# Optimization experiments

Hardware: AMD Instinct MI355X
Metric: run time of the kernel (lower is better)

Reference implementation:

```python
import jax, jax.numpy as jnp
import numpy as np

N_NODES = 50000
N_EDGES = 800000
HID = 64


def fake_quant_w(w):
    # symmetric per-tensor int8 fake quantization (num_bits=8)
    s = jnp.maximum(jnp.max(jnp.abs(w)) / 127.0, 1e-8)
    q = jnp.clip(jnp.round(w / s), -127.0, 127.0) * s
    return w + jax.lax.stop_gradient(q - w)


def layer_norm(x, g, b, eps=1e-5):
    mu = jnp.mean(x, axis=-1, keepdims=True)
    var = jnp.var(x, axis=-1, keepdims=True)
    return (x - mu) * jax.lax.rsqrt(var + eps) * g + b


def pointnet_conv(x, pos, src, dst, W, n_nodes):
    # message: cat([x_j, pos_j - pos_i]) @ W_q^T, max-aggregated at i (dst)
    rel = pos[src] - pos[dst]                       # [E, 3]
    feat = jnp.concatenate([x[src], rel], axis=-1)  # [E, C+3]
    msg = feat @ fake_quant_w(W).T                  # [E, 64]
    h = jax.ops.segment_max(msg, dst, num_segments=n_nodes)
    return jnp.where(jnp.isfinite(h), h, 0.0)       # empty segments -> 0


def setup_inputs() -> dict:
    key = jax.random.key(0)
    ks = jax.random.split(key, 16)
    d = {}
    d["x"] = jax.random.normal(ks[0], (N_NODES, 1), jnp.float32)
    d["pos"] = jax.random.normal(ks[1], (N_NODES, 3), jnp.float32)
    d["edge_index"] = jax.random.randint(ks[2], (2, N_EDGES), 0, N_NODES, jnp.int32)
    sc = 0.02
    d["W0"] = jax.random.normal(ks[3], (HID, 1 + 3), jnp.float32) * sc
    d["Ws"] = jax.random.normal(ks[4], (4, HID, HID + 3), jnp.float32) * sc
    d["ln_g"] = jnp.ones((5, HID), jnp.float32)
    d["ln_b"] = jnp.zeros((5, HID), jnp.float32)
    d["mlp_w1"] = jax.random.normal(ks[5], (128, 320), jnp.float32) * sc
    d["mlp_b1"] = jnp.zeros((128,), jnp.float32)
    d["mlp_w2"] = jax.random.normal(ks[6], (128, 128), jnp.float32) * sc
    d["mlp_b2"] = jnp.zeros((128,), jnp.float32)
    d["mlp_w3"] = jax.random.normal(ks[7], (64, 128), jnp.float32) * sc
    d["mlp_b3"] = jnp.zeros((64,), jnp.float32)
    d["mlp_w4"] = jax.random.normal(ks[8], (2, 64), jnp.float32) * sc
    d["mlp_b4"] = jnp.zeros((2,), jnp.float32)
    d["scale"] = jnp.ones((2,), jnp.float32)
    return d


def reference(x, pos, edge_index, W0, Ws, ln_g, ln_b,
              mlp_w1, mlp_b1, mlp_w2, mlp_b2, mlp_w3, mlp_b3, mlp_w4, mlp_b4,
              scale):
    src, dst = edge_index[0], edge_index[1]
    n = x.shape[0]
    embeddings = []
    h = x
    for i in range(5):
        W = W0 if i == 0 else Ws[i - 1]
        h = pointnet_conv(h, pos, src, dst, W, n)
        h = layer_norm(h, ln_g[i], ln_b[i])
        h = jax.nn.relu(h)
        embeddings.append(h)
    z = jnp.concatenate(embeddings, axis=-1)  # [N, 320]
    z = layer_norm(z, jnp.ones((z.shape[-1],), z.dtype), jnp.zeros((z.shape[-1],), z.dtype))
    z = jax.nn.relu(z @ mlp_w1.T + mlp_b1)
    z = jax.nn.relu(z @ mlp_w2.T + mlp_b2)
    z = jax.nn.relu(z @ mlp_w3.T + mlp_b3)
    flow = (z @ mlp_w4.T + mlp_b4) * scale
    return flow
```

## Files before the change

kernel.cpp:

```cpp
#include <hip/hip_runtime.h>
#include <hip/hip_bf16.h>

#define N_NODES 50000
#define N_EDGES 800000
#define NBLK 196

__device__ __forceinline__ float bf2f(unsigned short u) {
    union { unsigned int i; float f; } c; c.i = ((unsigned int)u) << 16; return c.f;
}
__device__ __forceinline__ unsigned short f2bf(float f) {
    union { float f; unsigned int u; } c; c.f = f;
    unsigned int u = c.u;
    u += 0x7fffu + ((u >> 16) & 1u);
    return (unsigned short)(u >> 16);
}
__device__ __forceinline__ float ldin(const void* p, long i, int f32) {
    return f32 ? ((const float*)p)[i] : bf2f(((const unsigned short*)p)[i]);
}
__device__ __forceinline__ float wsum(float v) {
#pragma unroll
    for (int m = 32; m; m >>= 1) v += __shfl_xor(v, m, 64);
    return v;
}

__global__ void probe_kernel(const unsigned short* __restrict__ lng, int* __restrict__ flag) {
    if (threadIdx.x == 0 && blockIdx.x == 0)
        flag[0] = (lng[0] == 0x3F80 && lng[1] == 0x3F80) ? 0 : 1;
}

__global__ __launch_bounds__(256) void hist_kernel(const int* __restrict__ ei, int* __restrict__ deg) {
    int e = blockIdx.x * 256 + threadIdx.x;
    if (e < N_EDGES) atomicAdd(&deg[ei[N_EDGES + e]], 1);
}

__global__ __launch_bounds__(256) void bsum_kernel(const int* __restrict__ deg,
                                                   int* __restrict__ bsum) {
    __shared__ int wt[4];
    const int t = threadIdx.x, lane = t & 63, wid = t >> 6;
    const int i = blockIdx.x * 256 + t;
    int v = (i < N_NODES) ? deg[i] : 0;
    int r = v;
#pragma unroll
    for (int m = 32; m; m >>= 1) r += __shfl_xor(r, m, 64);
    if (lane == 0) wt[wid] = r;
    __syncthreads();
    if (t == 0) bsum[blockIdx.x] = wt[0] + wt[1] + wt[2] + wt[3];
}

__global__ __launch_bounds__(256) void boff_kernel(const int* __restrict__ bsum,
                                                   int* __restrict__ boff) {
    __shared__ int wt[4];
    const int t = threadIdx.x, lane = t & 63, wid = t >> 6;
    int v = (t < NBLK) ? bsum[t] : 0;
    int inc = v;
#pragma unroll
    for (int off = 1; off < 64; off <<= 1) {
        int u = __shfl_up(inc, off, 64);
        if (lane >= off) inc += u;
    }
    if (lane == 63) wt[wid] = inc;
    __syncthreads();
    int woff = 0;
    for (int w = 0; w < wid; ++w) woff += wt[w];
    if (t < NBLK) boff[t] = inc - v + woff;
}

__global__ __launch_bounds__(256) void scanout_kernel(const int* __restrict__ deg,
                                                      const int* __restrict__ boff,
                                                      int* __restrict__ rowptr,
                                                      int* __restrict__ cursor) {
    __shared__ int wt[4];
    const int t = threadIdx.x, lane = t & 63, wid = t >> 6;
    const int i = blockIdx.x * 256 + t;
    int v = (i < N_NODES) ? deg[i] : 0;
    int inc = v;
#pragma unroll
    for (int off = 1; off < 64; off <<= 1) {
        int u = __shfl_up(inc, off, 64);
        if (lane >= off) inc += u;
    }
    if (lane == 63) wt[wid] = inc;
    __syncthreads();
    int woff = 0;
    for (int w = 0; w < wid; ++w) woff += wt[w];
    int excl = inc - v + woff + boff[blockIdx.x];
    if (i < N_NODES) {
        rowptr[i] = excl;
        cursor[i] = excl;
        if (i == N_NODES - 1) rowptr[N_NODES] = excl + v;
    }
}

__global__ __launch_bounds__(256) void scatter_kernel(const int* __restrict__ ei,
                                                      int* __restrict__ cursor,
                                                      int* __restrict__ csr_src) {
    int e = blockIdx.x * 256 + threadIdx.x;
    if (e < N_EDGES) {
        int src = ei[e];
        int dst = ei[N_EDGES + e];
        int p = atomicAdd(&cursor[dst], 1);
        csr_src[p] = src;
    }
}

__global__ __launch_bounds__(256) void quant_kernel(const void* __restrict__ W0,
                                                    const void* __restrict__ Ws,
                                                    float* __restrict__ Wc0,
                                                    float* __restrict__ Wc,
                                                    float* __restrict__ Wr,
                                                    const int* __restrict__ flagp) {
    const int f32 = *flagp;
    int layer = blockIdx.x;
    const void* src = (layer == 0) ? W0 : Ws;
    long sbase = (layer == 0) ? 0 : (long)(layer - 1) * 4288;
    float* dstc = (layer == 0) ? Wc0 : Wc + (size_t)(layer - 1) * 4352;
    float* dstr = (layer == 0) ? nullptr : Wr + (size_t)(layer - 1) * 4352;
    int Ki = (layer == 0) ? 4 : 67;
    int n = 64 * Ki;
    __shared__ float red[256];
    float amax = 0.0f;
    for (int i = threadIdx.x; i < n; i += 256) amax = fmaxf(amax, fabsf(ldin(src, sbase + i, f32)));
    red[threadIdx.x] = amax;
    __syncthreads();
    for (int s = 128; s > 0; s >>= 1) {
        if (threadIdx.x < s) red[threadIdx.x] = fmaxf(red[threadIdx.x], red[threadIdx.x + s]);
        __syncthreads();
    }
    float sc = fmaxf(red[0] / 127.0f, 1e-8f);
    for (int i = threadIdx.x; i < n; i += 256) {
        float w = ldin(src, sbase + i, f32);
        float q = rintf(w / sc);
        q = fminf(fmaxf(q, -127.0f), 127.0f);
        float v = q * sc;
        int o = i / Ki, k = i % Ki;
        dstc[(size_t)k * 64 + o] = v;
        if (dstr) dstr[(size_t)o * 68 + k] = v;
    }
}

__global__ __launch_bounds__(256) void wcvt_kernel(const void* __restrict__ w1,
                                                   const void* __restrict__ w2,
                                                   const void* __restrict__ w3,
                                                   float* __restrict__ Wm,
                                                   const int* __restrict__ flagp) {
    const int f32 = *flagp;
    const int i = blockIdx.x * 256 + threadIdx.x;
    if (i < 40960) Wm[i] = ldin(w1, i, f32);
    else if (i < 57344) Wm[i] = ldin(w2, i - 40960, f32);
    else if (i < 65536) Wm[i] = ldin(w3, i - 57344, f32);
}

__global__ __launch_bounds__(256) void u0_kernel(const void* __restrict__ x,
                                                 const void* __restrict__ pos,
                                                 const float* __restrict__ Wc0,
                                                 float* __restrict__ u,
                                                 const int* __restrict__ flagp) {
    const int f32 = *flagp;
    const int n = blockIdx.x * 256 + threadIdx.x;
    if (n >= N_NODES) return;
    const float xv = ldin(x, n, f32);
    const float p0 = ldin(pos, 3L * n + 0, f32);
    const float p1 = ldin(pos, 3L * n + 1, f32);
    const float p2 = ldin(pos, 3L * n + 2, f32);
    float4* up = reinterpret_cast<float4*>(u + (size_t)n * 64);
#pragma unroll
    for (int q = 0; q < 16; ++q) {
        const float4 w0 = *reinterpret_cast<const float4*>(Wc0 + 0 * 64 + 4 * q);
        const float4 w1 = *reinterpret_cast<const float4*>(Wc0 + 1 * 64 + 4 * q);
        const float4 w2 = *reinterpret_cast<const float4*>(Wc0 + 2 * 64 + 4 * q);
        const float4 w3 = *reinterpret_cast<const float4*>(Wc0 + 3 * 64 + 4 * q);
        float4 o;
        o.x = fmaf(p2, w3.x, fmaf(p1, w2.x, fmaf(p0, w1.x, xv * w0.x)));
        o.y = fmaf(p2, w3.y, fmaf(p1, w2.y, fmaf(p0, w1.y, xv * w0.y)));
        o.z = fmaf(p2, w3.z, fmaf(p1, w2.z, fmaf(p0, w1.z, xv * w0.z)));
        o.w = fmaf(p2, w3.w, fmaf(p1, w2.w, fmaf(p0, w1.w, xv * w0.w)));
        up[q] = o;
    }
}

__global__ __launch_bounds__(256) void agg_kernel(const float* __restrict__ u,
                                                  const void* __restrict__ pos,
                                                  const int* __restrict__ rowptr,
                                                  const int* __restrict__ csr,
                                                  const float* __restrict__ WcV, int vrow,
                                                  const void* __restrict__ lng,
                                                  const void* __restrict__ lnb,
                                                  int lnoff,
                                                  float* __restrict__ z, int out_off,
                                                  float2* __restrict__ stats,
                                                  const int* __restrict__ flagp) {
    const int f32 = *flagp;
    const int lane = threadIdx.x & 63;
    const int n = __builtin_amdgcn_readfirstlane((blockIdx.x * 256 + threadIdx.x) >> 6);
    if (n >= N_NODES) return;
    const int e0 = rowptr[n], e1 = rowptr[n + 1];
    float acc = -INFINITY;
    int e = e0;
    for (; e + 16 <= e1; e += 16) {
        float t0 = u[(size_t)csr[e + 0] * 64 + lane];
        float t1 = u[(size_t)csr[e + 1] * 64 + lane];
        float t2 = u[(size_t)csr[e + 2] * 64 + lane];
        float t3 = u[(size_t)csr[e + 3] * 64 + lane];
        float t4 = u[(size_t)csr[e + 4] * 64 + lane];
        float t5 = u[(size_t)csr[e + 5] * 64 + lane];
        float t6 = u[(size_t)csr[e + 6] * 64 + lane];
        float t7 = u[(size_t)csr[e + 7] * 64 + lane];
        float t8 = u[(size_t)csr[e + 8] * 64 + lane];
        float t9 = u[(size_t)csr[e + 9] * 64 + lane];
        float ta = u[(size_t)csr[e + 10] * 64 + lane];
        float tb = u[(size_t)csr[e + 11] * 64 + lane];
        float tc = u[(size_t)csr[e + 12] * 64 + lane];
        float td = u[(size_t)csr[e + 13] * 64 + lane];
        float te = u[(size_t)csr[e + 14] * 64 + lane];
        float tf = u[(size_t)csr[e + 15] * 64 + lane];
        float m0 = fmaxf(fmaxf(t0, t1), fmaxf(t2, t3));
        float m1 = fmaxf(fmaxf(t4, t5), fmaxf(t6, t7));
        float m2 = fmaxf(fmaxf(t8, t9), fmaxf(ta, tb));
        float m3 = fmaxf(fmaxf(tc, td), fmaxf(te, tf));
        acc = fmaxf(acc, fmaxf(fmaxf(m0, m1), fmaxf(m2, m3)));
    }
    for (; e + 4 <= e1; e += 4) {
        float t0 = u[(size_t)csr[e + 0] * 64 + lane];
        float t1 = u[(size_t)csr[e + 1] * 64 + lane];
        float t2 = u[(size_t)csr[e + 2] * 64 + lane];
        float t3 = u[(size_t)csr[e + 3] * 64 + lane];
        acc = fmaxf(acc, fmaxf(fmaxf(t0, t1), fmaxf(t2, t3)));
    }
    for (; e < e1; ++e)
        acc = fmaxf(acc, u[(size_t)csr[e] * 64 + lane]);
    const float p0 = ldin(pos, 3L * n + 0, f32);
    const float p1 = ldin(pos, 3L * n + 1, f32);
    const float p2 = ldin(pos, 3L * n + 2, f32);
    const float v = fmaf(p2, WcV[(size_t)(vrow + 2) * 64 + lane],
                    fmaf(p1, WcV[(size_t)(vrow + 1) * 64 + lane],
                         p0 * WcV[(size_t)(vrow + 0) * 64 + lane]));
    float h = acc - v;
    if (!isfinite(h)) h = 0.0f;
    const float g = ldin(lng, lnoff + lane, f32);
    const float bb = ldin(lnb, lnoff + lane, f32);
    const float mu = wsum(h) * (1.0f / 64.0f);
    const float dd = h - mu;
    const float var = wsum(dd * dd) * (1.0f / 64.0f);
    float y = dd * rsqrtf(var + 1e-5f) * g + bb;
    y = fmaxf(y, 0.0f);
    z[(size_t)n * 320 + out_off + lane] = y;
    if (stats) {
        const float* zr = z + (size_t)n * 320;
        const float v0 = zr[0 * 64 + lane];
        const float v1 = zr[1 * 64 + lane];
        const float v2 = zr[2 * 64 + lane];
        const float v3 = zr[3 * 64 + lane];
        const float s = ((v0 + v1) + (v2 + v3)) + y;
        const float mu2 = wsum(s) * (1.0f / 320.0f);
        float q = (v0 - mu2) * (v0 - mu2);
        q = fmaf(v1 - mu2, v1 - mu2, q);
        q = fmaf(v2 - mu2, v2 - mu2, q);
        q = fmaf(v3 - mu2, v3 - mu2, q);
        q = fmaf(y - mu2, y - mu2, q);
        const float var2 = wsum(q) * (1.0f / 320.0f);
        if (lane == 0) stats[n] = make_float2(mu2, rsqrtf(var2 + 1e-5f));
    }
}

__global__ __launch_bounds__(256) void un_kernel(const float* __restrict__ z, int in_off,
                                                 const float* __restrict__ Wr,
                                                 const void* __restrict__ pos,
                                                 float* __restrict__ un,
                                                 const int* __restrict__ flagp) {
    __shared__ float At[16][68];
    __shared__ float Wt[16][68];
    const int f32 = *flagp;
    const int tid = threadIdx.x;
    const int bn = blockIdx.x * 64;
    const int o_base = (tid & 15) * 4;
    const int n_base = (tid >> 4) * 4;
    const int sr = tid >> 2;
    const int kq = (tid & 3) * 4;
    float acc[4][4] = {};
    float4 av = make_float4(0.f, 0.f, 0.f, 0.f);
    if (bn + sr < N_NODES)
        av = *reinterpret_cast<const float4*>(z + (size_t)(bn + sr) * 320 + in_off + kq);
    float4 wv = *reinterpret_cast<const float4*>(Wr + (size_t)sr * 68 + kq);
    for (int kk = 0; kk < 64; kk += 16) {
        __syncthreads();
        At[kq + 0][sr] = av.x; At[kq + 1][sr] = av.y; At[kq + 2][sr] = av.z; At[kq + 3][sr] = av.w;
        Wt[kq + 0][sr] = wv.x; Wt[kq + 1][sr] = wv.y; Wt[kq + 2][sr] = wv.z; Wt[kq + 3][sr] = wv.w;
        __syncthreads();
        if (kk + 16 < 64) {
            av = make_float4(0.f, 0.f, 0.f, 0.f);
            if (bn + sr < N_NODES)
                av = *reinterpret_cast<const float4*>(z + (size_t)(bn + sr) * 320 + in_off + kk + 16 + kq);
            wv = *reinterpret_cast<const float4*>(Wr + (size_t)sr * 68 + kk + 16 + kq);
        }
#pragma unroll
        for (int k = 0; k < 16; ++k) {
            const float4 a4 = *reinterpret_cast<const float4*>(&At[k][n_base]);
            const float4 w4 = *reinterpret_cast<const float4*>(&Wt[k][o_base]);
            const float a[4] = { a4.x, a4.y, a4.z, a4.w };
            const float ww[4] = { w4.x, w4.y, w4.z, w4.w };
#pragma unroll
            for (int i = 0; i < 4; ++i)
#pragma unroll
                for (int j = 0; j < 4; ++j)
                    acc[i][j] = fmaf(a[i], ww[j], acc[i][j]);
        }
    }
    float wp[3][4];
#pragma unroll
    for (int c = 0; c < 3; ++c)
#pragma unroll
        for (int j = 0; j < 4; ++j)
            wp[c][j] = Wr[(size_t)(o_base + j) * 68 + 64 + c];
#pragma unroll
    for (int i = 0; i < 4; ++i) {
        const int n = bn + n_base + i;
        if (n < N_NODES) {
            const float p0 = ldin(pos, 3L * n + 0, f32);
            const float p1 = ldin(pos, 3L * n + 1, f32);
            const float p2 = ldin(pos, 3L * n + 2, f32);
#pragma unroll
            for (int j = 0; j < 4; ++j)
                un[(size_t)n * 64 + o_base + j] =
                    fmaf(p2, wp[2][j], fmaf(p1, wp[1][j], fmaf(p0, wp[0][j], acc[i][j])));
        }
    }
}

__global__ __launch_bounds__(256) void gemm128_kernel(const float* __restrict__ A,
                                                      const float* __restrict__ W,
                                                      const void* __restrict__ bias,
                                                      const float2* __restrict__ stats,
                                                      float* __restrict__ C,
                                                      int Ki,
                                                      const int* __restrict__ flagp) {
    __shared__ float At[16][68];
    __shared__ float Wt[16][132];
    const int f32 = *flagp;
    const int tid = threadIdx.x;
    const int bn = blockIdx.x * 64;
    const int sr = tid >> 2;
    const int kq = (tid & 3) * 4;
    const int wr = tid >> 1;
    const int kq2 = (tid & 1) * 8;
    const int n_base = (tid >> 4) * 4;
    const int o_base = (tid & 15) * 8;
    float mu = 0.f, rs = 1.f;
    if (stats && bn + sr < N_NODES) { float2 st = stats[bn + sr]; mu = st.x; rs = st.y; }
    float acc[4][8] = {};
    float4 av = make_float4(0.f, 0.f, 0.f, 0.f);
    if (bn + sr < N_NODES)
        av = *reinterpret_cast<const float4*>(A + (size_t)(bn + sr) * Ki + kq);
    float4 wv0 = *reinterpret_cast<const float4*>(W + (size_t)wr * Ki + kq2);
    float4 wv1 = *reinterpret_cast<const float4*>(W + (size_t)wr * Ki + kq2 + 4);
    for (int kk = 0; kk < Ki; kk += 16) {
        __syncthreads();
        At[kq + 0][sr] = (av.x - mu) * rs;
        At[kq + 1][sr] = (av.y - mu) * rs;
        At[kq + 2][sr] = (av.z - mu) * rs;
        At[kq + 3][sr] = (av.w - mu) * rs;
        Wt[kq2 + 0][wr] = wv0.x; Wt[kq2 + 1][wr] = wv0.y;
        Wt[kq2 + 2][wr] = wv0.z; Wt[kq2 + 3][wr] = wv0.w;
        Wt[kq2 + 4][wr] = wv1.x; Wt[kq2 + 5][wr] = wv1.y;
        Wt[kq2 + 6][wr] = wv1.z; Wt[kq2 + 7][wr] = wv1.w;
        __syncthreads();
        if (kk + 16 < Ki) {
            av = make_float4(0.f, 0.f, 0.f, 0.f);
            if (bn + sr < N_NODES)
                av = *reinterpret_cast<const float4*>(A + (size_t)(bn + sr) * Ki + kk + 16 + kq);
            wv0 = *reinterpret_cast<const float4*>(W + (size_t)wr * Ki + kk + 16 + kq2);
            wv1 = *reinterpret_cast<const float4*>(W + (size_t)wr * Ki + kk + 16 + kq2 + 4);
        }
#pragma unroll
        for (int k = 0; k < 16; ++k) {
            const float4 a4 = *reinterpret_cast<const float4*>(&At[k][n_base]);
            const float4 wa = *reinterpret_cast<const float4*>(&Wt[k][o_base]);
            const float4 wb = *reinterpret_cast<const float4*>(&Wt[k][o_base + 4]);
            const float a[4] = { a4.x, a4.y, a4.z, a4.w };
            const float ww[8] = { wa.x, wa.y, wa.z, wa.w, wb.x, wb.y, wb.z, wb.w };
#pragma unroll
            for (int i = 0; i < 4; ++i)
#pragma unroll
                for (int j = 0; j < 8; ++j)
                    acc[i][j] = fmaf(a[i], ww[j], acc[i][j]);
        }
    }
    float bj[8];
#pragma unroll
    for (int j = 0; j < 8; ++j) bj[j] = ldin(bias, o_base + j, f32);
#pragma unroll
    for (int i = 0; i < 4; ++i) {
        const int n = bn + n_base + i;
        if (n < N_NODES) {
            float4 c0, c1;
            c0.x = fmaxf(acc[i][0] + bj[0], 0.f); c0.y = fmaxf(acc[i][1] + bj[1], 0.f);
            c0.z = fmaxf(acc[i][2] + bj[2], 0.f); c0.w = fmaxf(acc[i][3] + bj[3], 0.f);
            c1.x = fmaxf(acc[i][4] + bj[4], 0.f); c1.y = fmaxf(acc[i][5] + bj[5], 0.f);
            c1.z = fmaxf(acc[i][6] + bj[6], 0.f); c1.w = fmaxf(acc[i][7] + bj[7], 0.f);
            *reinterpret_cast<float4*>(C + (size_t)n * 128 + o_base) = c0;
            *reinterpret_cast<float4*>(C + (size_t)n * 128 + o_base + 4) = c1;
        }
    }
}

__global__ __launch_bounds__(256) void gemm64out_kernel(const float* __restrict__ A,
                                                        const float* __restrict__ W,
                                                        const void* __restrict__ bias,
                                                        const void* __restrict__ w4,
                                                        const void* __restrict__ b4,
                                                        const void* __restrict__ scale,
                                                        void* __restrict__ out,
                                                        const int* __restrict__ flagp) {
    __shared__ float At[16][68];
    __shared__ float Wt[16][68];
    __shared__ float h3t[64][65];
    const int f32 = *flagp;
    const int tid = threadIdx.x;
    const int bn = blockIdx.x * 64;
    const int Ki = 128;
    const int o_base = (tid & 15) * 4;
    const int n_base = (tid >> 4) * 4;
    const int sr = tid >> 2;
    const int kq = (tid & 3) * 4;
    float acc[4][4] = {};
    float4 av = make_float4(0.f, 0.f, 0.f, 0.f);
    if (bn + sr < N_NODES)
        av = *reinterpret_cast<const float4*>(A + (size_t)(bn + sr) * Ki + kq);
    float4 wv = *reinterpret_cast<const float4*>(W + (size_t)sr * Ki + kq);
    for (int kk = 0; kk < Ki; kk += 16) {
        __syncthreads();
        At[kq + 0][sr] = av.x; At[kq + 1][sr] = av.y; At[kq + 2][sr] = av.z; At[kq + 3][sr] = av.w;
        Wt[kq + 0][sr] = wv.x; Wt[kq + 1][sr] = wv.y; Wt[kq + 2][sr] = wv.z; Wt[kq + 3][sr] = wv.w;
        __syncthreads();
        if (kk + 16 < Ki) {
            av = make_float4(0.f, 0.f, 0.f, 0.f);
            if (bn + sr < N_NODES)
                av = *reinterpret_cast<const float4*>(A + (size_t)(bn + sr) * Ki + kk + 16 + kq);
            wv = *reinterpret_cast<const float4*>(W + (size_t)sr * Ki + kk + 16 + kq);
        }
#pragma unroll
        for (int k = 0; k < 16; ++k) {
            const float4 a4 = *reinterpret_cast<const float4*>(&At[k][n_base]);
            const float4 w4v = *reinterpret_cast<const float4*>(&Wt[k][o_base]);
            const float a[4] = { a4.x, a4.y, a4.z, a4.w };
            const float ww[4] = { w4v.x, w4v.y, w4v.z, w4v.w };
#pragma unroll
            for (int i = 0; i < 4; ++i)
#pragma unroll
                for (int j = 0; j < 4; ++j)
                    acc[i][j] = fmaf(a[i], ww[j], acc[i][j]);
        }
    }
    float bj[4];
#pragma unroll
    for (int j = 0; j < 4; ++j) bj[j] = ldin(bias, o_base + j, f32);
    __syncthreads();
#pragma unroll
    for (int i = 0; i < 4; ++i)
#pragma unroll
        for (int j = 0; j < 4; ++j)
            h3t[n_base + i][o_base + j] = fmaxf(acc[i][j] + bj[j], 0.f);
    __syncthreads();
    const int lane = tid & 63, wid = tid >> 6;
    const float wa = ldin(w4, lane, f32);
    const float wb = ldin(w4, 64 + lane, f32);
    const float b0 = ldin(b4, 0, f32), b1 = ldin(b4, 1, f32);
    const float s0 = ldin(scale, 0, f32), s1 = ldin(scale, 1, f32);
#pragma unroll
    for (int r = wid * 16; r < wid * 16 + 16; ++r) {
        const int n = bn + r;
        if (n >= N_NODES) break;
        const float hv = h3t[r][lane];
        const float d0 = wsum(hv * wa);
        const float d1 = wsum(hv * wb);
        if (lane == 0) {
            const float o0 = (d0 + b0) * s0;
            const float o1 = (d1 + b1) * s1;
            if (f32) {
                ((float*)out)[n * 2 + 0] = o0;
                ((float*)out)[n * 2 + 1] = o1;
            } else {
                ((unsigned short*)out)[n * 2 + 0] = f2bf(o0);
                ((unsigned short*)out)[n * 2 + 1] = f2bf(o1);
            }
        }
    }
}

extern "C" void kernel_launch(void* const* d_in, const int* in_sizes, int n_in,
                              void* d_out, int out_size, void* d_ws, size_t ws_size,
                              hipStream_t stream) {
    (void)in_sizes; (void)n_in; (void)out_size; (void)ws_size;
    const void* x    = d_in[0];
    const void* pos  = d_in[1];
    const int*  ei   = (const int*)d_in[2];
    const void* W0   = d_in[3];
    const void* Ws   = d_in[4];
    const void* lng  = d_in[5];
    const void* lnb  = d_in[6];
    const void* w1   = d_in[7];
    const void* b1   = d_in[8];
    const void* w2   = d_in[9];
    const void* b2   = d_in[10];
    const void* w3   = d_in[11];
    const void* b3   = d_in[12];
    const void* w4   = d_in[13];
    const void* b4   = d_in[14];
    const void* scl  = d_in[15];

    float* z      = (float*)d_ws;
    float* h1     = z + 16000000;
    float* Wc0    = h1 + 6400000;
    float* Wc     = Wc0 + 256;
    float* Wr     = Wc + 17408;
    float* Wm     = Wr + 17408;
    int*   deg    = (int*)(Wm + 65536);
    int*   rowptr = deg + N_NODES;
    int*   cursor = rowptr + (N_NODES + 1);
    int*   flag   = cursor + N_NODES;
    int*   csr    = flag + 1;
    int*   bsum   = csr + N_EDGES;
    int*   boff   = bsum + 256;
    float2* stats = (float2*)(boff + 256);
    float* Wm1 = Wm, *Wm2 = Wm + 40960, *Wm3 = Wm + 57344;
    float* ua     = h1;
    float* ub     = h1 + 3200000;
    float* h2 = z;

    hipMemsetAsync(deg, 0, N_NODES * sizeof(int), stream);
    probe_kernel<<<1, 64, 0, stream>>>((const unsigned short*)lng, flag);
    hist_kernel<<<(N_EDGES + 255) / 256, 256, 0, stream>>>(ei, deg);
    bsum_kernel<<<NBLK, 256, 0, stream>>>(deg, bsum);
    boff_kernel<<<1, 256, 0, stream>>>(bsum, boff);
    scanout_kernel<<<NBLK, 256, 0, stream>>>(deg, boff, rowptr, cursor);
    scatter_kernel<<<(N_EDGES + 255) / 256, 256, 0, stream>>>(ei, cursor, csr);
    quant_kernel<<<5, 256, 0, stream>>>(W0, Ws, Wc0, Wc, Wr, flag);
    wcvt_kernel<<<256, 256, 0, stream>>>(w1, w2, w3, Wm, flag);

    const int gagg = (N_NODES * 64 + 255) / 256;
    const int gun  = (N_NODES + 63) / 64;

    u0_kernel<<<NBLK, 256, 0, stream>>>(x, pos, Wc0, ua, flag);
    agg_kernel<<<gagg, 256, 0, stream>>>(ua, pos, rowptr, csr, Wc0, 1,
                                         lng, lnb, 0, z, 0, nullptr, flag);
    un_kernel<<<gun, 256, 0, stream>>>(z, 0, Wr + 0 * 4352, pos, ub, flag);
    agg_kernel<<<gagg, 256, 0, stream>>>(ub, pos, rowptr, csr, Wc + 0 * 4352, 64,
                                         lng, lnb, 64, z, 64, nullptr, flag);
    un_kernel<<<gun, 256, 0, stream>>>(z, 64, Wr + 1 * 4352, pos, ua, flag);
    agg_kernel<<<gagg, 256, 0, stream>>>(ua, pos, rowptr, csr, Wc + 1 * 4352, 64,
                                         lng, lnb, 128, z, 128, nullptr, flag);
    un_kernel<<<gun, 256, 0, stream>>>(z, 128, Wr + 2 * 4352, pos, ub, flag);
    agg_kernel<<<gagg, 256, 0, stream>>>(ub, pos, rowptr, csr, Wc + 2 * 4352, 64,
                                         lng, lnb, 192, z, 192, nullptr, flag);
    un_kernel<<<gun, 256, 0, stream>>>(z, 192, Wr + 3 * 4352, pos, ua, flag);
    agg_kernel<<<gagg, 256, 0, stream>>>(ua, pos, rowptr, csr, Wc + 3 * 4352, 64,
                                         lng, lnb, 256, z, 256, stats, flag);

    const int gg = (N_NODES + 63) / 64;
    gemm128_kernel<<<gg, 256, 0, stream>>>(z, Wm1, b1, stats, h1, 320, flag);
    gemm128_kernel<<<gg, 256, 0, stream>>>(h1, Wm2, b2, nullptr, h2, 128, flag);
    gemm64out_kernel<<<gg, 256, 0, stream>>>(h2, Wm3, b3, w4, b4, scl, d_out, flag);
}
```

Measured before the change: 571.3 us.

## Fuse three MLP GEMMs into one kernel with shared-memory intermediates; merge prep kernels

```diff
diff --git a/kernel.cpp b/kernel.cpp
--- a/kernel.cpp
+++ b/kernel.cpp
@@ -14,6 +14,10 @@
     u += 0x7fffu + ((u >> 16) & 1u);
     return (unsigned short)(u >> 16);
 }
+__device__ __forceinline__ int is_f32(const void* lng) {
+    const unsigned short* p = (const unsigned short*)lng;
+    return !(p[0] == 0x3F80 && p[1] == 0x3F80);
+}
 __device__ __forceinline__ float ldin(const void* p, long i, int f32) {
     return f32 ? ((const float*)p)[i] : bf2f(((const unsigned short*)p)[i]);
 }
@@ -21,11 +25,6 @@
 #pragma unroll
     for (int m = 32; m; m >>= 1) v += __shfl_xor(v, m, 64);
     return v;
-}
-
-__global__ void probe_kernel(const unsigned short* __restrict__ lng, int* __restrict__ flag) {
-    if (threadIdx.x == 0 && blockIdx.x == 0)
-        flag[0] = (lng[0] == 0x3F80 && lng[1] == 0x3F80) ? 0 : 1;
 }
 
 __global__ __launch_bounds__(256) void hist_kernel(const int* __restrict__ ei, int* __restrict__ deg) {
@@ -103,13 +102,24 @@
     }
 }
 
-__global__ __launch_bounds__(256) void quant_kernel(const void* __restrict__ W0,
-                                                    const void* __restrict__ Ws,
-                                                    float* __restrict__ Wc0,
-                                                    float* __restrict__ Wc,
-                                                    float* __restrict__ Wr,
-                                                    const int* __restrict__ flagp) {
-    const int f32 = *flagp;
+__global__ __launch_bounds__(256) void prep_kernel(const void* __restrict__ W0,
+                                                   const void* __restrict__ Ws,
+                                                   const void* __restrict__ w1,
+                                                   const void* __restrict__ w2,
+                                                   const void* __restrict__ w3,
+                                                   float* __restrict__ Wc0,
+                                                   float* __restrict__ Wc,
+                                                   float* __restrict__ Wr,
+                                                   float* __restrict__ Wm,
+                                                   const void* __restrict__ lng) {
+    const int f32 = is_f32(lng);
+    if (blockIdx.x >= 5) {
+        const int i = (blockIdx.x - 5) * 256 + threadIdx.x;
+        if (i < 40960) Wm[i] = ldin(w1, i, f32);
+        else if (i < 57344) Wm[i] = ldin(w2, i - 40960, f32);
+        else if (i < 65536) Wm[i] = ldin(w3, i - 57344, f32);
+        return;
+    }
     int layer = blockIdx.x;
     const void* src = (layer == 0) ? W0 : Ws;
     long sbase = (layer == 0) ? 0 : (long)(layer - 1) * 4288;
@@ -138,24 +148,12 @@
     }
 }
 
-__global__ __launch_bounds__(256) void wcvt_kernel(const void* __restrict__ w1,
-                                                   const void* __restrict__ w2,
-                                                   const void* __restrict__ w3,
-                                                   float* __restrict__ Wm,
-                                                   const int* __restrict__ flagp) {
-    const int f32 = *flagp;
-    const int i = blockIdx.x * 256 + threadIdx.x;
-    if (i < 40960) Wm[i] = ldin(w1, i, f32);
-    else if (i < 57344) Wm[i] = ldin(w2, i - 40960, f32);
-    else if (i < 65536) Wm[i] = ldin(w3, i - 57344, f32);
-}
-
 __global__ __launch_bounds__(256) void u0_kernel(const void* __restrict__ x,
                                                  const void* __restrict__ pos,
                                                  const float* __restrict__ Wc0,
                                                  float* __restrict__ u,
-                                                 const int* __restrict__ flagp) {
-    const int f32 = *flagp;
+                                                 const void* __restrict__ lng) {
+    const int f32 = is_f32(lng);
     const int n = blockIdx.x * 256 + threadIdx.x;
     if (n >= N_NODES) return;
     const float xv = ldin(x, n, f32);
@@ -187,9 +185,8 @@
                                                   const void* __restrict__ lnb,
                                                   int lnoff,
                                                   float* __restrict__ z, int out_off,
-                                                  float2* __restrict__ stats,
-                                                  const int* __restrict__ flagp) {
-    const int f32 = *flagp;
+                                                  float2* __restrict__ stats) {
+    const int f32 = is_f32(lng);
     const int lane = threadIdx.x & 63;
     const int n = __builtin_amdgcn_readfirstlane((blockIdx.x * 256 + threadIdx.x) >> 6);
     if (n >= N_NODES) return;
@@ -266,10 +263,10 @@
                                                  const float* __restrict__ Wr,
                                                  const void* __restrict__ pos,
                                                  float* __restrict__ un,
-                                                 const int* __restrict__ flagp) {
+                                                 const void* __restrict__ lng) {
     __shared__ float At[16][68];
     __shared__ float Wt[16][68];
-    const int f32 = *flagp;
+    const int f32 = is_f32(lng);
     const int tid = threadIdx.x;
     const int bn = blockIdx.x * 64;
     const int o_base = (tid & 15) * 4;
@@ -326,155 +323,183 @@
     }
 }
 
-__global__ __launch_bounds__(256) void gemm128_kernel(const float* __restrict__ A,
-                                                      const float* __restrict__ W,
-                                                      const void* __restrict__ bias,
-                                                      const float2* __restrict__ stats,
-                                                      float* __restrict__ C,
-                                                      int Ki,
-                                                      const int* __restrict__ flagp) {
-    __shared__ float At[16][68];
+__global__ __launch_bounds__(256) void mlp_kernel(const float* __restrict__ z,
+                                                  const float* __restrict__ Wm,
+                                                  const void* __restrict__ b1,
+                                                  const void* __restrict__ b2,
+                                                  const void* __restrict__ b3,
+                                                  const float2* __restrict__ stats,
+                                                  const void* __restrict__ w4,
+                                                  const void* __restrict__ b4,
+                                                  const void* __restrict__ scale,
+                                                  void* __restrict__ out,
+                                                  const void* __restrict__ lng) {
+    __shared__ float At[16][36];
     __shared__ float Wt[16][132];
-    const int f32 = *flagp;
+    __shared__ float h1t[128][33];
+    __shared__ float h2t[128][33];
+    __shared__ float h3t[64][33];
+    const int f32 = is_f32(lng);
     const int tid = threadIdx.x;
-    const int bn = blockIdx.x * 64;
-    const int sr = tid >> 2;
-    const int kq = (tid & 3) * 4;
-    const int wr = tid >> 1;
+    const int bn = blockIdx.x * 32;
+    const int sr1 = tid >> 3;
+    const int kq1 = (tid & 7) * 2;
+    const int wr  = tid >> 1;
     const int kq2 = (tid & 1) * 8;
-    const int n_base = (tid >> 4) * 4;
-    const int o_base = (tid & 15) * 8;
+    const int n_base = (tid >> 4) * 2;
+    const int o_base = (tid & 15) * 4;
+    const float* W1 = Wm;
+    const float* W2 = Wm + 40960;
+    const float* W3 = Wm + 57344;
+
     float mu = 0.f, rs = 1.f;
-    if (stats && bn + sr < N_NODES) { float2 st = stats[bn + sr]; mu = st.x; rs = st.y; }
-    float acc[4][8] = {};
-    float4 av = make_float4(0.f, 0.f, 0.f, 0.f);
-    if (bn + sr < N_NODES)
-        av = *reinterpret_cast<const float4*>(A + (size_t)(bn + sr) * Ki + kq);
-    float4 wv0 = *reinterpret_cast<const float4*>(W + (size_t)wr * Ki + kq2);
-    float4 wv1 = *reinterpret_cast<const float4*>(W + (size_t)wr * Ki + kq2 + 4);
-    for (int kk = 0; kk < Ki; kk += 16) {
-        __syncthreads();
-        At[kq + 0][sr] = (av.x - mu) * rs;
-        At[kq + 1][sr] = (av.y - mu) * rs;
-        At[kq + 2][sr] = (av.z - mu) * rs;
-        At[kq + 3][sr] = (av.w - mu) * rs;
+    if (bn + sr1 < N_NODES) { float2 st = stats[bn + sr1]; mu = st.x; rs = st.y; }
+
+    float acc[2][8] = {};
+    float2 av = make_float2(0.f, 0.f);
+    if (bn + sr1 < N_NODES)
+        av = *reinterpret_cast<const float2*>(z + (size_t)(bn + sr1) * 320 + kq1);
+    float4 wv0 = *reinterpret_cast<const float4*>(W1 + (size_t)wr * 320 + kq2);
+    float4 wv1 = *reinterpret_cast<const float4*>(W1 + (size_t)wr * 320 + kq2 + 4);
+    for (int kk = 0; kk < 320; kk += 16) {
+        __syncthreads();
+        At[kq1 + 0][sr1] = (av.x - mu) * rs;
+        At[kq1 + 1][sr1] = (av.y - mu) * rs;
         Wt[kq2 + 0][wr] = wv0.x; Wt[kq2 + 1][wr] = wv0.y;
         Wt[kq2 + 2][wr] = wv0.z; Wt[kq2 + 3][wr] = wv0.w;
         Wt[kq2 + 4][wr] = wv1.x; Wt[kq2 + 5][wr] = wv1.y;
         Wt[kq2 + 6][wr] = wv1.z; Wt[kq2 + 7][wr] = wv1.w;
         __syncthreads();
-        if (kk + 16 < Ki) {
-            av = make_float4(0.f, 0.f, 0.f, 0.f);
-            if (bn + sr < N_NODES)
-                av = *reinterpret_cast<const float4*>(A + (size_t)(bn + sr) * Ki + kk + 16 + kq);
-            wv0 = *reinterpret_cast<const float4*>(W + (size_t)wr * Ki + kk + 16 + kq2);
-            wv1 = *reinterpret_cast<const float4*>(W + (size_t)wr * Ki + kk + 16 + kq2 + 4);
+        if (kk + 16 < 320) {
+            av = make_float2(0.f, 0.f);
+            if (bn + sr1 < N_NODES)
+                av = *reinterpret_cast<const float2*>(z + (size_t)(bn + sr1) * 320 + kk + 16 + kq1);
+            wv0 = *reinterpret_cast<const float4*>(W1 + (size_t)wr * 320 + kk + 16 + kq2);
+            wv1 = *reinterpret_cast<const float4*>(W1 + (size_t)wr * 320 + kk + 16 + kq2 + 4);
         }
 #pragma unroll
         for (int k = 0; k < 16; ++k) {
-            const float4 a4 = *reinterpret_cast<const float4*>(&At[k][n_base]);
+            const float2 a2 = *reinterpret_cast<const float2*>(&At[k][n_base]);
             const float4 wa = *reinterpret_cast<const float4*>(&Wt[k][o_base]);
-            const float4 wb = *reinterpret_cast<const float4*>(&Wt[k][o_base + 4]);
-            const float a[4] = { a4.x, a4.y, a4.z, a4.w };
-            const float ww[8] = { wa.x, wa.y, wa.z, wa.w, wb.x, wb.y, wb.z, wb.w };
-#pragma unroll
-            for (int i = 0; i < 4; ++i)
+            const float4 wb = *reinterpret_cast<const float4*>(&Wt[k][64 + o_base]);
+            const float a[2] = { a2.x, a2.y };
+            const float w8[8] = { wa.x, wa.y, wa.z, wa.w, wb.x, wb.y, wb.z, wb.w };
+#pragma unroll
+            for (int i = 0; i < 2; ++i)
 #pragma unroll
                 for (int j = 0; j < 8; ++j)
-                    acc[i][j] = fmaf(a[i], ww[j], acc[i][j]);
-        }
-    }
-    float bj[8];
-#pragma unroll
-    for (int j = 0; j < 8; ++j) bj[j] = ldin(bias, o_base + j, f32);
-#pragma unroll
-    for (int i = 0; i < 4; ++i) {
-        const int n = bn + n_base + i;
-        if (n < N_NODES) {
-            float4 c0, c1;
-            c0.x = fmaxf(acc[i][0] + bj[0], 0.f); c0.y = fmaxf(acc[i][1] + bj[1], 0.f);
-            c0.z = fmaxf(acc[i][2] + bj[2], 0.f); c0.w = fmaxf(acc[i][3] + bj[3], 0.f);
-            c1.x = fmaxf(acc[i][4] + bj[4], 0.f); c1.y = fmaxf(acc[i][5] + bj[5], 0.f);
-            c1.z = fmaxf(acc[i][6] + bj[6], 0.f); c1.w = fmaxf(acc[i][7] + bj[7], 0.f);
-            *reinterpret_cast<float4*>(C + (size_t)n * 128 + o_base) = c0;
-            *reinterpret_cast<float4*>(C + (size_t)n * 128 + o_base + 4) = c1;
-        }
-    }
-}
-
-__global__ __launch_bounds__(256) void gemm64out_kernel(const float* __restrict__ A,
-                                                        const float* __restrict__ W,
-                                                        const void* __restrict__ bias,
-                                                        const void* __restrict__ w4,
-                                                        const void* __restrict__ b4,
-                                                        const void* __restrict__ scale,
-                                                        void* __restrict__ out,
-                                                        const int* __restrict__ flagp) {
-    __shared__ float At[16][68];
-    __shared__ float Wt[16][68];
-    __shared__ float h3t[64][65];
-    const int f32 = *flagp;
-    const int tid = threadIdx.x;
-    const int bn = blockIdx.x * 64;
-    const int Ki = 128;
-    const int o_base = (tid & 15) * 4;
-    const int n_base = (tid >> 4) * 4;
-    const int sr = tid >> 2;
-    const int kq = (tid & 3) * 4;
-    float acc[4][4] = {};
-    float4 av = make_float4(0.f, 0.f, 0.f, 0.f);
-    if (bn + sr < N_NODES)
-        av = *reinterpret_cast<const float4*>(A + (size_t)(bn + sr) * Ki + kq);
-    float4 wv = *reinterpret_cast<const float4*>(W + (size_t)sr * Ki + kq);
-    for (int kk = 0; kk < Ki; kk += 16) {
-        __syncthreads();
-        At[kq + 0][sr] = av.x; At[kq + 1][sr] = av.y; At[kq + 2][sr] = av.z; At[kq + 3][sr] = av.w;
-        Wt[kq + 0][sr] = wv.x; Wt[kq + 1][sr] = wv.y; Wt[kq + 2][sr] = wv.z; Wt[kq + 3][sr] = wv.w;
-        __syncthreads();
-        if (kk + 16 < Ki) {
-            av = make_float4(0.f, 0.f, 0.f, 0.f);
-            if (bn + sr < N_NODES)
-                av = *reinterpret_cast<const float4*>(A + (size_t)(bn + sr) * Ki + kk + 16 + kq);
-            wv = *reinterpret_cast<const float4*>(W + (size_t)sr * Ki + kk + 16 + kq);
+                    acc[i][j] = fmaf(a[i], w8[j], acc[i][j]);
+        }
+    }
+    {
+        float bj[8];
+#pragma unroll
+        for (int j = 0; j < 4; ++j) {
+            bj[j]     = ldin(b1, o_base + j, f32);
+            bj[4 + j] = ldin(b1, 64 + o_base + j, f32);
+        }
+#pragma unroll
+        for (int i = 0; i < 2; ++i)
+#pragma unroll
+            for (int j = 0; j < 4; ++j) {
+                h1t[o_base + j][n_base + i]      = fmaxf(acc[i][j] + bj[j], 0.f);
+                h1t[64 + o_base + j][n_base + i] = fmaxf(acc[i][4 + j] + bj[4 + j], 0.f);
+            }
+    }
+    float acc2[2][8] = {};
+    wv0 = *reinterpret_cast<const float4*>(W2 + (size_t)wr * 128 + kq2);
+    wv1 = *reinterpret_cast<const float4*>(W2 + (size_t)wr * 128 + kq2 + 4);
+    for (int kk = 0; kk < 128; kk += 16) {
+        __syncthreads();
+        Wt[kq2 + 0][wr] = wv0.x; Wt[kq2 + 1][wr] = wv0.y;
+        Wt[kq2 + 2][wr] = wv0.z; Wt[kq2 + 3][wr] = wv0.w;
+        Wt[kq2 + 4][wr] = wv1.x; Wt[kq2 + 5][wr] = wv1.y;
+        Wt[kq2 + 6][wr] = wv1.z; Wt[kq2 + 7][wr] = wv1.w;
+        __syncthreads();
+        if (kk + 16 < 128) {
+            wv0 = *reinterpret_cast<const float4*>(W2 + (size_t)wr * 128 + kk + 16 + kq2);
+            wv1 = *reinterpret_cast<const float4*>(W2 + (size_t)wr * 128 + kk + 16 + kq2 + 4);
         }
 #pragma unroll
         for (int k = 0; k < 16; ++k) {
-            const float4 a4 = *reinterpret_cast<const float4*>(&At[k][n_base]);
-            const float4 w4v = *reinterpret_cast<const float4*>(&Wt[k][o_base]);
-            const float a[4] = { a4.x, a4.y, a4.z, a4.w };
-            const float ww[4] = { w4v.x, w4v.y, w4v.z, w4v.w };
-#pragma unroll
-            for (int i = 0; i < 4; ++i)
-#pragma unroll
-                for (int j = 0; j < 4; ++j)
-                    acc[i][j] = fmaf(a[i], ww[j], acc[i][j]);
-        }
-    }
-    float bj[4];
-#pragma unroll
-    for (int j = 0; j < 4; ++j) bj[j] = ldin(bias, o_base + j, f32);
-    __syncthreads();
-#pragma unroll
-    for (int i = 0; i < 4; ++i)
-#pragma unroll
-        for (int j = 0; j < 4; ++j)
-            h3t[n_base + i][o_base + j] = fmaxf(acc[i][j] + bj[j], 0.f);
+            const float2 a2 = *reinterpret_cast<const float2*>(&h1t[kk + k][n_base]);
+            const float4 wa = *reinterpret_cast<const float4*>(&Wt[k][o_base]);
+            const float4 wb = *reinterpret_cast<const float4*>(&Wt[k][64 + o_base]);
+            const float a[2] = { a2.x, a2.y };
+            const float w8[8] = { wa.x, wa.y, wa.z, wa.w, wb.x, wb.y, wb.z, wb.w };
+#pragma unroll
+            for (int i = 0; i < 2; ++i)
+#pragma unroll
+                for (int j = 0; j < 8; ++j)
+                    acc2[i][j] = fmaf(a[i], w8[j], acc2[i][j]);
+        }
+    }
+    {
+        float bj[8];
+#pragma unroll
+        for (int j = 0; j < 4; ++j) {
+            bj[j]     = ldin(b2, o_base + j, f32);
+            bj[4 + j] = ldin(b2, 64 + o_base + j, f32);
+        }
+#pragma unroll
+        for (int i = 0; i < 2; ++i)
+#pragma unroll
+            for (int j = 0; j < 4; ++j) {
+                h2t[o_base + j][n_base + i]      = fmaxf(acc2[i][j] + bj[j], 0.f);
+                h2t[64 + o_base + j][n_base + i] = fmaxf(acc2[i][4 + j] + bj[4 + j], 0.f);
+            }
+    }
+    const int wr3 = tid >> 2;
+    const int kq3 = (tid & 3) * 4;
+    float acc3[2][4] = {};
+    float4 wv3 = *reinterpret_cast<const float4*>(W3 + (size_t)wr3 * 128 + kq3);
+    for (int kk = 0; kk < 128; kk += 16) {
+        __syncthreads();
+        Wt[kq3 + 0][wr3] = wv3.x; Wt[kq3 + 1][wr3] = wv3.y;
+        Wt[kq3 + 2][wr3] = wv3.z; Wt[kq3 + 3][wr3] = wv3.w;
+        __syncthreads();
+        if (kk + 16 < 128)
+            wv3 = *reinterpret_cast<const float4*>(W3 + (size_t)wr3 * 128 + kk + 16 + kq3);
+#pragma unroll
+        for (int k = 0; k < 16; ++k) {
+            const float2 a2 = *reinterpret_cast<const float2*>(&h2t[kk + k][n_base]);
+            const float4 wa = *reinterpret_cast<const float4*>(&Wt[k][o_base]);
+            const float a[2] = { a2.x, a2.y };
+#pragma unroll
+            for (int i = 0; i < 2; ++i) {
+                acc3[i][0] = fmaf(a[i], wa.x, acc3[i][0]);
+                acc3[i][1] = fmaf(a[i], wa.y, acc3[i][1]);
+                acc3[i][2] = fmaf(a[i], wa.z, acc3[i][2]);
+                acc3[i][3] = fmaf(a[i], wa.w, acc3[i][3]);
+            }
+        }
+    }
+    {
+        float bj[4];
+#pragma unroll
+        for (int j = 0; j < 4; ++j) bj[j] = ldin(b3, o_base + j, f32);
+#pragma unroll
+        for (int i = 0; i < 2; ++i)
+#pragma unroll
+            for (int j = 0; j < 4; ++j)
+                h3t[o_base + j][n_base + i] = fmaxf(acc3[i][j] + bj[j], 0.f);
+    }
     __syncthreads();
     const int lane = tid & 63, wid = tid >> 6;
     const float wa = ldin(w4, lane, f32);
     const float wb = ldin(w4, 64 + lane, f32);
-    const float b0 = ldin(b4, 0, f32), b1 = ldin(b4, 1, f32);
+    const float c0 = ldin(b4, 0, f32), c1 = ldin(b4, 1, f32);
     const float s0 = ldin(scale, 0, f32), s1 = ldin(scale, 1, f32);
 #pragma unroll
-    for (int r = wid * 16; r < wid * 16 + 16; ++r) {
+    for (int r = wid * 8; r < wid * 8 + 8; ++r) {
         const int n = bn + r;
         if (n >= N_NODES) break;
-        const float hv = h3t[r][lane];
+        const float hv = h3t[lane][r];
         const float d0 = wsum(hv * wa);
         const float d1 = wsum(hv * wb);
         if (lane == 0) {
-            const float o0 = (d0 + b0) * s0;
-            const float o1 = (d1 + b1) * s1;
+            const float o0 = (d0 + c0) * s0;
+            const float o1 = (d1 + c1) * s1;
             if (f32) {
                 ((float*)out)[n * 2 + 0] = o0;
                 ((float*)out)[n * 2 + 1] = o1;
@@ -508,55 +533,48 @@
     const void* scl  = d_in[15];
 
     float* z      = (float*)d_ws;
-    float* h1     = z + 16000000;
-    float* Wc0    = h1 + 6400000;
+    float* ua     = z + 16000000;
+    float* ub     = ua + 3200000;
+    float* Wc0    = ub + 3200000;
     float* Wc     = Wc0 + 256;
     float* Wr     = Wc + 17408;
     float* Wm     = Wr + 17408;
     int*   deg    = (int*)(Wm + 65536);
     int*   rowptr = deg + N_NODES;
     int*   cursor = rowptr + (N_NODES + 1);
-    int*   flag   = cursor + N_NODES;
-    int*   csr    = flag + 1;
+    int*   csr    = cursor + N_NODES;
     int*   bsum   = csr + N_EDGES;
     int*   boff   = bsum + 256;
     float2* stats = (float2*)(boff + 256);
-    float* Wm1 = Wm, *Wm2 = Wm + 40960, *Wm3 = Wm + 57344;
-    float* ua     = h1;
-    float* ub     = h1 + 3200000;
-    float* h2 = z;
 
     hipMemsetAsync(deg, 0, N_NODES * sizeof(int), stream);
-    probe_kernel<<<1, 64, 0, stream>>>((const unsigned short*)lng, flag);
     hist_kernel<<<(N_EDGES + 255) / 256, 256, 0, stream>>>(ei, deg);
     bsum_kernel<<<NBLK, 256, 0, stream>>>(deg, bsum);
     boff_kernel<<<1, 256, 0, stream>>>(bsum, boff);
     scanout_kernel<<<NBLK, 256, 0, stream>>>(deg, boff, rowptr, cursor);
     scatter_kernel<<<(N_EDGES + 255) / 256, 256, 0, stream>>>(ei, cursor, csr);
-    quant_kernel<<<5, 256, 0, stream>>>(W0, Ws, Wc0, Wc, Wr, flag);
-    wcvt_kernel<<<256, 256, 0, stream>>>(w1, w2, w3, Wm, flag);
+    prep_kernel<<<261, 256, 0, stream>>>(W0, Ws, w1, w2, w3, Wc0, Wc, Wr, Wm, lng);
 
     const int gagg = (N_NODES * 64 + 255) / 256;
     const int gun  = (N_NODES + 63) / 64;
 
-    u0_kernel<<<NBLK, 256, 0, stream>>>(x, pos, Wc0, ua, flag);
+    u0_kernel<<<NBLK, 256, 0, stream>>>(x, pos, Wc0, ua, lng);
     agg_kernel<<<gagg, 256, 0, stream>>>(ua, pos, rowptr, csr, Wc0, 1,
-                                         lng, lnb, 0, z, 0, nullptr, flag);
-    un_kernel<<<gun, 256, 0, stream>>>(z, 0, Wr + 0 * 4352, pos, ub, flag);
+                                         lng, lnb, 0, z, 0, nullptr);
+    un_kernel<<<gun, 256, 0, stream>>>(z, 0, Wr + 0 * 4352, pos, ub, lng);
     agg_kernel<<<gagg, 256, 0, stream>>>(ub, pos, rowptr, csr, Wc + 0 * 4352, 64,
-                                         lng, lnb, 64, z, 64, nullptr, flag);
-    un_kernel<<<gun, 256, 0, stream>>>(z, 64, Wr + 1 * 4352, pos, ua, flag);
+                                         lng, lnb, 64, z, 64, nullptr);
+    un_kernel<<<gun, 256, 0, stream>>>(z, 64, Wr + 1 * 4352, pos, ua, lng);
     agg_kernel<<<gagg, 256, 0, stream>>>(ua, pos, rowptr, csr, Wc + 1 * 4352, 64,
-                                         lng, lnb, 128, z, 128, nullptr, flag);
-    un_kernel<<<gun, 256, 0, stream>>>(z, 128, Wr + 2 * 4352, pos, ub, flag);
+                                         lng, lnb, 128, z, 128, nullptr);
+    un_kernel<<<gun, 256, 0, stream>>>(z, 128, Wr + 2 * 4352, pos, ub, lng);
     agg_kernel<<<gagg, 256, 0, stream>>>(ub, pos, rowptr, csr, Wc + 2 * 4352, 64,
-                                         lng, lnb, 192, z, 192, nullptr, flag);
-    un_kernel<<<gun, 256, 0, stream>>>(z, 192, Wr + 3 * 4352, pos, ua, flag);
+                                         lng, lnb, 192, z, 192, nullptr);
+    un_kernel<<<gun, 256, 0, stream>>>(z, 192, Wr + 3 * 4352, pos, ua, lng);
     agg_kernel<<<gagg, 256, 0, stream>>>(ua, pos, rowptr, csr, Wc + 3 * 4352, 64,
-                                         lng, lnb, 256, z, 256, stats, flag);
-
-    const int gg = (N_NODES + 63) / 64;
-    gemm128_kernel<<<gg, 256, 0, stream>>>(z, Wm1, b1, stats, h1, 320, flag);
-    gemm128_kernel<<<gg, 256, 0, stream>>>(h1, Wm2, b2, nullptr, h2, 128, flag);
-    gemm64out_kernel<<<gg, 256, 0, stream>>>(h2, Wm3, b3, w4, b4, scl, d_out, flag);
-}
+                                         lng, lnb, 256, z, 256, stats);
+
+    const int gmlp = (N_NODES + 31) / 32;
+    mlp_kernel<<<gmlp, 256, 0, stream>>>(z, Wm, b1, b2, b3, stats,
+                                         w4, b4, scl, d_out, lng);
+}
```

Measured after the change: 593.1 us. 1.04x slower.
